# Kernel tuning notes

Hardware: AMD Instinct MI355X
Metric: run time of the kernel (lower is better)

Reference implementation:

```python
import jax, jax.numpy as jnp
import numpy as np

N_E = 1024
E_DIM = 256
N_TOK = 131072


def setup_inputs() -> dict:
    key = jax.random.key(0)
    kz, kw = jax.random.split(key)
    z = jax.random.normal(kz, (N_TOK, E_DIM), dtype=jnp.float32)
    weight = jax.random.normal(kw, (N_E, E_DIM), dtype=jnp.float32)
    return {"z": z, "weight": weight}


def reference(z, weight):
    # squared L2 distances: ||z||^2 + ||e||^2 - 2 z e^T  -> [N, n_e]
    d = (jnp.sum(z * z, axis=1, keepdims=True)
         + jnp.sum(weight * weight, axis=1)
         - 2.0 * jnp.matmul(z, weight.T))
    idx = jnp.argmin(d, axis=1)                       # [N]
    # gather codebook rows instead of materializing the one-hot @ weight matmul
    z_q = weight[idx]                                 # [N, e_dim]
    # straight-through estimator
    z_q = z + jax.lax.stop_gradient(z_q - z)
    # e_mean = mean of one-hot encodings == normalized code counts
    counts = jax.ops.segment_sum(jnp.ones_like(idx, dtype=z.dtype), idx,
                                 num_segments=N_E)    # [n_e]
    e_mean = counts / z.shape[0]
    perplexity = jnp.exp(-jnp.sum(e_mean * jnp.log(e_mean + 1e-10)))
    return z_q, perplexity
```

## Files before the change

kernel.cpp:

```cpp
#include <hip/hip_runtime.h>
#include <math.h>

#define NE   1024
#define ED   256
#define NT   131072
#define SLOTS 32

typedef __attribute__((ext_vector_type(8))) short short8;
typedef __attribute__((ext_vector_type(4))) float f32x4;

__device__ inline unsigned short f2bf(float f) {
    unsigned u = __float_as_uint(f);
    unsigned r = (u + 0x7FFFu + ((u >> 16) & 1u)) >> 16;
    return (unsigned short)r;
}

__device__ inline void gl_lds16(const void* g, void* l) {
    __builtin_amdgcn_global_load_lds(
        (const __attribute__((address_space(1))) unsigned int*)g,
        (__attribute__((address_space(3))) unsigned int*)l, 16, 0, 0);
}

__device__ inline unsigned pack_cand(float s, int code) {
    float qf = (s + 1024.f) * 16.f;
    int q = (int)qf;
    q = q < 0 ? 0 : (q > 65535 ? 65535 : q);
    return ((unsigned)q << 16) | (unsigned)code;
}


__global__ __launch_bounds__(256) void vq_prep(const float* __restrict__ w,
                                               float* __restrict__ wnorm,
                                               int* __restrict__ counts,
                                               unsigned short* __restrict__ wb) {
    int c = blockIdx.x * 256 + threadIdx.x;
    if (c < NE) {
        const float4* row = reinterpret_cast<const float4*>(w + (size_t)c * ED);
        ushort4* wbr = reinterpret_cast<ushort4*>(wb + (size_t)c * ED);
        float s = 0.f;
#pragma unroll 8
        for (int i = 0; i < ED / 4; ++i) {
            float4 v = row[i];
            s += v.x * v.x + v.y * v.y + v.z * v.z + v.w * v.w;
            ushort4 o;
            o.x = f2bf(v.x); o.y = f2bf(v.y); o.z = f2bf(v.z); o.w = f2bf(v.w);
            wbr[i] = o;
        }
        wnorm[c] = s;
        counts[c] = 0;
    }
}

__global__ __launch_bounds__(1024) void vq_wmax(const float* __restrict__ wnorm,
                                                float* __restrict__ wmax) {
    __shared__ float red[16];
    int tid = threadIdx.x;
    float v = wnorm[tid];
#pragma unroll
    for (int m = 32; m >= 1; m >>= 1) v = fmaxf(v, __shfl_xor(v, m, 64));
    if ((tid & 63) == 0) red[tid >> 6] = v;
    __syncthreads();
    if (tid == 0) {
        float m = red[0];
#pragma unroll
        for (int i = 1; i < 16; ++i) m = fmaxf(m, red[i]);
        wmax[0] = sqrtf(m);
    }
}

__global__ __launch_bounds__(512, 2) void vq_score3(const float* __restrict__ z,
                                                    const unsigned short* __restrict__ wb,
                                                    const float* __restrict__ wnorm,
                                                    const float* __restrict__ wmaxp,
                                                    unsigned* __restrict__ cnt,
                                                    unsigned* __restrict__ cand) {
    __shared__ __align__(16) unsigned short wlds[32768];
    __shared__ float wn_lds[NE];
    __shared__ float thr_lds[8][32];

    const int tid  = threadIdx.x;
    const int lane = tid & 63;
    const int wv_  = tid >> 6;
    const int l15  = lane & 15;
    const int l4   = lane >> 4;
    const int row0 = blockIdx.x * 256 + wv_ * 32;

#pragma unroll
    for (int p = 0; p < 8; ++p) {
        int s  = wv_ * 8 + p;
        int nj = s >> 3, kg = s & 7;
        int j  = nj * 16 + l15;
        gl_lds16(wb + (size_t)j * ED + kg * 32 + l4 * 8, &wlds[s * 512]);
    }

    reinterpret_cast<float2*>(wn_lds)[tid] = reinterpret_cast<const float2*>(wnorm)[tid];

    short8 a[2][8];
    float zn2[2];
#pragma unroll
    for (int mi = 0; mi < 2; ++mi) {
        const float* zr = z + (size_t)(row0 + mi * 16 + l15) * ED;
        float s = 0.f;
#pragma unroll
        for (int kg = 0; kg < 8; ++kg) {
            int k0 = kg * 32 + l4 * 8;
            float4 p = *reinterpret_cast<const float4*>(zr + k0);
            float4 q = *reinterpret_cast<const float4*>(zr + k0 + 4);
            s += p.x * p.x + p.y * p.y + p.z * p.z + p.w * p.w
               + q.x * q.x + q.y * q.y + q.z * q.z + q.w * q.w;
            short8 t;
            t[0] = (short)f2bf(p.x); t[1] = (short)f2bf(p.y);
            t[2] = (short)f2bf(p.z); t[3] = (short)f2bf(p.w);
            t[4] = (short)f2bf(q.x); t[5] = (short)f2bf(q.y);
            t[6] = (short)f2bf(q.z); t[7] = (short)f2bf(q.w);
            a[mi][kg] = t;
        }
        zn2[mi] = s;
    }
#pragma unroll
    for (int mi = 0; mi < 2; ++mi) {
        zn2[mi] += __shfl_xor(zn2[mi], 16, 64);
        zn2[mi] += __shfl_xor(zn2[mi], 32, 64);
    }
    float wmax = wmaxp[0];
#pragma unroll
    for (int mi = 0; mi < 2; ++mi)
        thr_lds[wv_][mi * 16 + l15] = 0.0313f * sqrtf(zn2[mi]) * wmax + 0.05f;

    asm volatile("s_waitcnt vmcnt(0) lgkmcnt(0)" ::: "memory");
    __builtin_amdgcn_s_barrier();

    float thrR[2], mn[2];
    int cnt_reg[2];
#pragma unroll
    for (int mi = 0; mi < 2; ++mi) {
        thrR[mi] = thr_lds[wv_][mi * 16 + l15];
        mn[mi] = 3.4e38f;
        cnt_reg[mi] = 0;
    }

    for (int st = 0; st < 8; ++st) {
        const int c0 = st * 128;

        for (int base = 0; base < 8; base += 2) {
            f32x4 acc[2][2];
#pragma unroll
            for (int tb = 0; tb < 2; ++tb)
#pragma unroll
                for (int mi = 0; mi < 2; ++mi) acc[tb][mi] = {0.f, 0.f, 0.f, 0.f};

#pragma unroll
            for (int tb = 0; tb < 2; ++tb)
#pragma unroll
                for (int kg = 0; kg < 8; ++kg) {
                    short8 wf = *reinterpret_cast<const short8*>(
                        &wlds[(((base + tb) * 8 + kg) * 512) + lane * 8]);
                    acc[tb][0] = __builtin_amdgcn_mfma_f32_16x16x32_bf16(wf, a[0][kg], acc[tb][0], 0, 0, 0);
                    acc[tb][1] = __builtin_amdgcn_mfma_f32_16x16x32_bf16(wf, a[1][kg], acc[tb][1], 0, 0, 0);
                }

            float4 wnv[2];
#pragma unroll
            for (int tb = 0; tb < 2; ++tb)
                wnv[tb] = *reinterpret_cast<const float4*>(
                    &wn_lds[c0 + (base + tb) * 16 + l4 * 4]);

            float tmin[2] = {3.4e38f, 3.4e38f};
#pragma unroll
            for (int tb = 0; tb < 2; ++tb)
#pragma unroll
                for (int mi = 0; mi < 2; ++mi) {
                    float wr[4] = {wnv[tb].x, wnv[tb].y, wnv[tb].z, wnv[tb].w};
#pragma unroll
                    for (int r = 0; r < 4; ++r) {
                        float s = fmaf(-2.f, acc[tb][mi][r], wr[r]);
                        acc[tb][mi][r] = s;
                        tmin[mi] = fminf(tmin[mi], s);
                    }
                }
#pragma unroll
            for (int mi = 0; mi < 2; ++mi) {
                float v = tmin[mi];
                v = fminf(v, __shfl_xor(v, 16, 64));
                v = fminf(v, __shfl_xor(v, 32, 64));
                mn[mi] = fminf(mn[mi], v);
            }

            unsigned km[2] = {0u, 0u};
#pragma unroll
            for (int tb = 0; tb < 2; ++tb)
#pragma unroll
                for (int mi = 0; mi < 2; ++mi)
#pragma unroll
                    for (int r = 0; r < 4; ++r)
                        if (acc[tb][mi][r] <= mn[mi] + thrR[mi])
                            km[mi] |= 1u << (tb * 4 + r);

            if (__any((km[0] | km[1]) != 0u)) {
#pragma unroll
                for (int mi = 0; mi < 2; ++mi) {
                    int kc = __popc(km[mi]);
                    int b = __shfl_xor(kc, 16, 64);
                    int c = __shfl_xor(kc, 32, 64);
                    int d = __shfl_xor(b, 32, 64);
                    int tot = kc + b + c + d;
                    if (tot > 0) {
                        int pfx = (l4 == 1) ? b
                                : (l4 == 2) ? (c + d)
                                : (l4 == 3) ? (b + c + d) : 0;
                        int tok = row0 + mi * 16 + l15;
                        int o = 0;
#pragma unroll
                        for (int tb = 0; tb < 2; ++tb)
#pragma unroll
                            for (int r = 0; r < 4; ++r)
                                if (km[mi] & (1u << (tb * 4 + r))) {
                                    int pos = cnt_reg[mi] + pfx + o;
                                    if (pos < SLOTS)
                                        cand[(size_t)tok * SLOTS + pos] =
                                            pack_cand(acc[tb][mi][r],
                                                      c0 + (base + tb) * 16 + l4 * 4 + r);
                                    ++o;
                                }
                        cnt_reg[mi] += tot;
                    }
                }
            }
        }

        if (st < 7) {
            asm volatile("s_waitcnt lgkmcnt(0)" ::: "memory");
            __builtin_amdgcn_s_barrier();
#pragma unroll
            for (int p = 0; p < 8; ++p) {
                int s  = wv_ * 8 + p;
                int nj = s >> 3, kg = s & 7;
                int j  = (st + 1) * 128 + nj * 16 + l15;
                gl_lds16(wb + (size_t)j * ED + kg * 32 + l4 * 8, &wlds[s * 512]);
            }
            asm volatile("s_waitcnt vmcnt(0) lgkmcnt(0)" ::: "memory");
            __builtin_amdgcn_s_barrier();
        }
    }

    if (l4 == 0) {
        cnt[row0 + l15]      = (unsigned)cnt_reg[0];
        cnt[row0 + 16 + l15] = (unsigned)cnt_reg[1];
    }
}

__global__ __launch_bounds__(256) void vq_refine(const float* __restrict__ z,
                                                 const float* __restrict__ w,
                                                 const float* __restrict__ wnorm,
                                                 const float* __restrict__ wmaxp,
                                                 const unsigned* __restrict__ cnt,
                                                 const unsigned* __restrict__ cand,
                                                 int* __restrict__ counts,
                                                 float* __restrict__ out) {
    const int lane = threadIdx.x & 63;
    const int t = blockIdx.x * 4 + (threadIdx.x >> 6);
    float4 zv = reinterpret_cast<const float4*>(z + (size_t)t * ED)[lane];
    unsigned n = cnt[t];
    float bs = 3.4e38f;
    int bj = NE;

    if (n >= 1u && n <= (unsigned)SLOTS) {
        unsigned pk = 0xFFFFFFFFu;
        if (lane < (int)n) pk = cand[(size_t)t * SLOTS + lane];
        unsigned pmin = pk;
#pragma unroll
        for (int m = 1; m < 64; m <<= 1) {
            unsigned o = __shfl_xor(pmin, m, 64);
            pmin = o < pmin ? o : pmin;
        }
        float zn = zv.x * zv.x + zv.y * zv.y + zv.z * zv.z + zv.w * zv.w;
#pragma unroll
        for (int m = 1; m < 64; m <<= 1) zn += __shfl_xor(zn, m, 64);
        float thr = 0.0313f * sqrtf(zn) * wmaxp[0] + 0.05f;
        unsigned margin = (unsigned)(16.f * thr) + 2u;
        unsigned qmin = pmin >> 16;
        bool keep = (lane < (int)n) && ((pk >> 16) <= qmin + margin);
        unsigned long long mask = __ballot(keep);
        while (mask) {
            int c = __ffsll(mask) - 1;
            mask &= mask - 1;
            int j = (int)(__shfl(pk, c, 64) & 0xFFFFu);
            float4 wv = reinterpret_cast<const float4*>(w + (size_t)j * ED)[lane];
            float d = fmaf(zv.x, wv.x, fmaf(zv.y, wv.y, fmaf(zv.z, wv.z, zv.w * wv.w)));
#pragma unroll
            for (int m = 1; m < 64; m <<= 1) d += __shfl_xor(d, m, 64);
            float s = fmaf(-2.f, d, wnorm[j]);
            if (s < bs || (s == bs && j < bj)) { bs = s; bj = j; }
        }
    } else {
        for (int j = 0; j < NE; ++j) {
            float4 wv = reinterpret_cast<const float4*>(w + (size_t)j * ED)[lane];
            float d = fmaf(zv.x, wv.x, fmaf(zv.y, wv.y, fmaf(zv.z, wv.z, zv.w * wv.w)));
#pragma unroll
            for (int m = 1; m < 64; m <<= 1) d += __shfl_xor(d, m, 64);
            float s = fmaf(-2.f, d, wnorm[j]);
            if (s < bs || (s == bs && j < bj)) { bs = s; bj = j; }
        }
    }
    float4 bw = reinterpret_cast<const float4*>(w + (size_t)bj * ED)[lane];
    reinterpret_cast<float4*>(out + (size_t)t * ED)[lane] = bw;
    if (lane == 0) atomicAdd(&counts[bj], 1);
}

__global__ __launch_bounds__(1024) void vq_pplx(const int* __restrict__ counts,
                                                float* __restrict__ out) {
    __shared__ float red[16];
    int tid = threadIdx.x;
    float e = (float)counts[tid] * (1.0f / (float)NT);
    float t = -e * logf(e + 1e-10f);
#pragma unroll
    for (int m = 32; m >= 1; m >>= 1) t += __shfl_down(t, m, 64);
    if ((tid & 63) == 0) red[tid >> 6] = t;
    __syncthreads();
    if (tid < 16) {
        float s = red[tid];
#pragma unroll
        for (int m = 8; m >= 1; m >>= 1) s += __shfl_down(s, m, 16);
        if (tid == 0) out[(size_t)NT * ED] = expf(s);
    }
}

#define TM 64
#define TN 64
#define KC 64

__global__ __launch_bounds__(256) void vq_prep0(const float* __restrict__ w,
                                                float* __restrict__ wnorm,
                                                int* __restrict__ counts) {
    int c = blockIdx.x * blockDim.x + threadIdx.x;
    if (c < NE) {
        const float4* row = reinterpret_cast<const float4*>(w + (size_t)c * ED);
        float s = 0.f;
#pragma unroll 8
        for (int i = 0; i < ED / 4; ++i) {
            float4 v = row[i];
            s += v.x * v.x + v.y * v.y + v.z * v.z + v.w * v.w;
        }
        wnorm[c] = s;
        counts[c] = 0;
    }
}

__global__ __launch_bounds__(256) void vq_argmin0(const float* __restrict__ z,
                                                  const float* __restrict__ w,
                                                  const float* __restrict__ wnorm,
                                                  int* __restrict__ idx_out,
                                                  int* __restrict__ counts) {
    __shared__ float zs[ED][TM];
    __shared__ float wsh[KC][TN];
    const int tid  = threadIdx.x;
    const int row0 = blockIdx.x * TM;
    const int cg   = tid & 15;
    const int tg   = tid >> 4;
#pragma unroll
    for (int p = 0; p < 16; ++p) {
        int f = p * 256 + tid;
        int k = f >> 4;
        int g = f & 15;
        float4 v;
        v.x = z[(size_t)(row0 + g * 4 + 0) * ED + k];
        v.y = z[(size_t)(row0 + g * 4 + 1) * ED + k];
        v.z = z[(size_t)(row0 + g * 4 + 2) * ED + k];
        v.w = z[(size_t)(row0 + g * 4 + 3) * ED + k];
        *reinterpret_cast<float4*>(&zs[k][g * 4]) = v;
    }
    float best[4];
    int   bidx[4];
#pragma unroll
    for (int i = 0; i < 4; ++i) { best[i] = 3.4e38f; bidx[i] = 0; }
    for (int ct = 0; ct < NE / TN; ++ct) {
        const int c0 = ct * TN;
        float acc[4][4];
#pragma unroll
        for (int i = 0; i < 4; ++i)
#pragma unroll
            for (int j = 0; j < 4; ++j) acc[i][j] = 0.f;
        for (int kc = 0; kc < ED / KC; ++kc) {
            __syncthreads();
#pragma unroll
            for (int p = 0; p < 4; ++p) {
                int f = p * 256 + tid;
                int k = f >> 4;
                int g = f & 15;
                float4 v;
                v.x = w[(size_t)(c0 + g * 4 + 0) * ED + kc * KC + k];
                v.y = w[(size_t)(c0 + g * 4 + 1) * ED + kc * KC + k];
                v.z = w[(size_t)(c0 + g * 4 + 2) * ED + kc * KC + k];
                v.w = w[(size_t)(c0 + g * 4 + 3) * ED + kc * KC + k];
                *reinterpret_cast<float4*>(&wsh[k][g * 4]) = v;
            }
            __syncthreads();
#pragma unroll 8
            for (int k = 0; k < KC; ++k) {
                float4 zv = *reinterpret_cast<const float4*>(&zs[kc * KC + k][tg * 4]);
                float4 wv = *reinterpret_cast<const float4*>(&wsh[k][cg * 4]);
                float zr[4] = { zv.x, zv.y, zv.z, zv.w };
                float wr[4] = { wv.x, wv.y, wv.z, wv.w };
#pragma unroll
                for (int i = 0; i < 4; ++i)
#pragma unroll
                    for (int j = 0; j < 4; ++j)
                        acc[i][j] = fmaf(zr[i], wr[j], acc[i][j]);
            }
        }
#pragma unroll
        for (int j = 0; j < 4; ++j) {
            int c = c0 + cg * 4 + j;
            float wn = wnorm[c];
#pragma unroll
            for (int i = 0; i < 4; ++i) {
                float s = fmaf(-2.f, acc[i][j], wn);
                if (s < best[i]) { best[i] = s; bidx[i] = c; }
            }
        }
    }
#pragma unroll
    for (int m = 1; m < 16; m <<= 1) {
#pragma unroll
        for (int i = 0; i < 4; ++i) {
            float ov = __shfl_xor(best[i], m, 64);
            int   oi = __shfl_xor(bidx[i], m, 64);
            if (ov < best[i] || (ov == best[i] && oi < bidx[i])) {
                best[i] = ov; bidx[i] = oi;
            }
        }
    }
    if (cg == 0) {
#pragma unroll
        for (int i = 0; i < 4; ++i) {
            int t = row0 + tg * 4 + i;
            idx_out[t] = bidx[i];
            atomicAdd(&counts[bidx[i]], 1);
        }
    }
}

__global__ __launch_bounds__(256) void vq_gather0(const float* __restrict__ w,
                                                  const int* __restrict__ idx,
                                                  float* __restrict__ out) {
    int tid = threadIdx.x;
    int t   = blockIdx.x * 4 + (tid >> 6);
    int c4  = tid & 63;
    int id  = idx[t];
    float4 v = reinterpret_cast<const float4*>(w + (size_t)id * ED)[c4];
    reinterpret_cast<float4*>(out + (size_t)t * ED)[c4] = v;
}

extern "C" void kernel_launch(void* const* d_in, const int* in_sizes, int n_in,
                              void* d_out, int out_size, void* d_ws, size_t ws_size,
                              hipStream_t stream) {
    const float* z = (const float*)d_in[0];
    const float* w = (const float*)d_in[1];
    float* out = (float*)d_out;
    char* ws = (char*)d_ws;

    float*          wnorm  = (float*)ws;
    int*            counts = (int*)(ws + 4096);
    float*          wmax   = (float*)(ws + 8192);
    unsigned short* wb     = (unsigned short*)(ws + 8448);
    unsigned*       cnt    = (unsigned*)(ws + 532736);
    unsigned*       cand   = (unsigned*)(ws + 1057024);
    const size_t need = 1057024 + (size_t)NT * SLOTS * 4;

    if (ws_size >= need) {
        vq_prep<<<4, 256, 0, stream>>>(w, wnorm, counts, wb);
        vq_wmax<<<1, 1024, 0, stream>>>(wnorm, wmax);
        vq_score3<<<NT / 256, 512, 0, stream>>>(z, wb, wnorm, wmax, cnt, cand);
        vq_refine<<<NT / 4, 256, 0, stream>>>(z, w, wnorm, wmax, cnt, cand, counts, out);
        vq_pplx<<<1, 1024, 0, stream>>>(counts, out);
    } else {
        int* idxw = (int*)(ws + 8192);
        vq_prep0<<<(NE + 255) / 256, 256, 0, stream>>>(w, wnorm, counts);
        vq_argmin0<<<NT / TM, 256, 0, stream>>>(z, w, wnorm, idxw, counts);
        vq_gather0<<<NT / 4, 256, 0, stream>>>(w, idxw, out);
        vq_pplx<<<1, 1024, 0, stream>>>(counts, out);
    }
}
```

Before: 281.6 us.

## Drop LDS staging of codebook; read bf16 weights directly into registers

The scoring kernel no longer stages codebook tiles in LDS with barriers. Each wave now loads its MFMA B-fragments straight from global memory, relying on L2 and L1 caching since the bf16 codebook is small. Each wave also handles 64 tokens instead of 32, so every loaded weight fragment feeds four MFMAs, and blocks shrink to 256 threads. This removes LDS traffic and block-wide synchronisation. In exchange it adds global and L1 load latency on the critical path and higher register pressure from 32 A-fragments per lane.

```diff
diff --git a/kernel.cpp b/kernel.cpp
--- a/kernel.cpp
+++ b/kernel.cpp
@@ -13,12 +13,6 @@
     unsigned u = __float_as_uint(f);
     unsigned r = (u + 0x7FFFu + ((u >> 16) & 1u)) >> 16;
     return (unsigned short)r;
-}
-
-__device__ inline void gl_lds16(const void* g, void* l) {
-    __builtin_amdgcn_global_load_lds(
-        (const __attribute__((address_space(1))) unsigned int*)g,
-        (__attribute__((address_space(3))) unsigned int*)l, 16, 0, 0);
 }
 
 __device__ inline unsigned pack_cand(float s, int code) {
@@ -68,184 +62,159 @@
     }
 }
 
-__global__ __launch_bounds__(512, 2) void vq_score3(const float* __restrict__ z,
-                                                    const unsigned short* __restrict__ wb,
-                                                    const float* __restrict__ wnorm,
-                                                    const float* __restrict__ wmaxp,
-                                                    unsigned* __restrict__ cnt,
-                                                    unsigned* __restrict__ cand) {
-    __shared__ __align__(16) unsigned short wlds[32768];
-    __shared__ float wn_lds[NE];
-    __shared__ float thr_lds[8][32];
-
+__global__ __launch_bounds__(256) void vq_score4(const float* __restrict__ z,
+                                                 const unsigned short* __restrict__ wb,
+                                                 const float* __restrict__ wnorm,
+                                                 const float* __restrict__ wmaxp,
+                                                 unsigned* __restrict__ cnt,
+                                                 unsigned* __restrict__ cand) {
     const int tid  = threadIdx.x;
     const int lane = tid & 63;
     const int wv_  = tid >> 6;
     const int l15  = lane & 15;
     const int l4   = lane >> 4;
-    const int row0 = blockIdx.x * 256 + wv_ * 32;
-
-#pragma unroll
-    for (int p = 0; p < 8; ++p) {
-        int s  = wv_ * 8 + p;
-        int nj = s >> 3, kg = s & 7;
-        int j  = nj * 16 + l15;
-        gl_lds16(wb + (size_t)j * ED + kg * 32 + l4 * 8, &wlds[s * 512]);
-    }
-
-    reinterpret_cast<float2*>(wn_lds)[tid] = reinterpret_cast<const float2*>(wnorm)[tid];
-
-    short8 a[2][8];
-    float zn2[2];
-#pragma unroll
-    for (int mi = 0; mi < 2; ++mi) {
-        const float* zr = z + (size_t)(row0 + mi * 16 + l15) * ED;
-        float s = 0.f;
-#pragma unroll
-        for (int kg = 0; kg < 8; ++kg) {
-            int k0 = kg * 32 + l4 * 8;
-            float4 p = *reinterpret_cast<const float4*>(zr + k0);
-            float4 q = *reinterpret_cast<const float4*>(zr + k0 + 4);
-            s += p.x * p.x + p.y * p.y + p.z * p.z + p.w * p.w
-               + q.x * q.x + q.y * q.y + q.z * q.z + q.w * q.w;
-            short8 t;
-            t[0] = (short)f2bf(p.x); t[1] = (short)f2bf(p.y);
-            t[2] = (short)f2bf(p.z); t[3] = (short)f2bf(p.w);
-            t[4] = (short)f2bf(q.x); t[5] = (short)f2bf(q.y);
-            t[6] = (short)f2bf(q.z); t[7] = (short)f2bf(q.w);
-            a[mi][kg] = t;
-        }
-        zn2[mi] = s;
-    }
-#pragma unroll
-    for (int mi = 0; mi < 2; ++mi) {
-        zn2[mi] += __shfl_xor(zn2[mi], 16, 64);
-        zn2[mi] += __shfl_xor(zn2[mi], 32, 64);
-    }
-    float wmax = wmaxp[0];
-#pragma unroll
-    for (int mi = 0; mi < 2; ++mi)
-        thr_lds[wv_][mi * 16 + l15] = 0.0313f * sqrtf(zn2[mi]) * wmax + 0.05f;
-
-    asm volatile("s_waitcnt vmcnt(0) lgkmcnt(0)" ::: "memory");
-    __builtin_amdgcn_s_barrier();
-
-    float thrR[2], mn[2];
-    int cnt_reg[2];
-#pragma unroll
-    for (int mi = 0; mi < 2; ++mi) {
-        thrR[mi] = thr_lds[wv_][mi * 16 + l15];
-        mn[mi] = 3.4e38f;
-        cnt_reg[mi] = 0;
-    }
-
-    for (int st = 0; st < 8; ++st) {
-        const int c0 = st * 128;
-
-        for (int base = 0; base < 8; base += 2) {
-            f32x4 acc[2][2];
-#pragma unroll
-            for (int tb = 0; tb < 2; ++tb)
-#pragma unroll
-                for (int mi = 0; mi < 2; ++mi) acc[tb][mi] = {0.f, 0.f, 0.f, 0.f};
-
-#pragma unroll
-            for (int tb = 0; tb < 2; ++tb)
-#pragma unroll
-                for (int kg = 0; kg < 8; ++kg) {
-                    short8 wf = *reinterpret_cast<const short8*>(
-                        &wlds[(((base + tb) * 8 + kg) * 512) + lane * 8]);
-                    acc[tb][0] = __builtin_amdgcn_mfma_f32_16x16x32_bf16(wf, a[0][kg], acc[tb][0], 0, 0, 0);
-                    acc[tb][1] = __builtin_amdgcn_mfma_f32_16x16x32_bf16(wf, a[1][kg], acc[tb][1], 0, 0, 0);
+    const int row0 = blockIdx.x * 256 + wv_ * 64;
+
+    short8 a[4][8];
+    float thrR[4], mn[4];
+    int cnt_reg[4];
+    {
+        float wmax = wmaxp[0];
+#pragma unroll
+        for (int mi = 0; mi < 4; ++mi) {
+            const float* zr = z + (size_t)(row0 + mi * 16 + l15) * ED;
+            float s = 0.f;
+#pragma unroll
+            for (int kg = 0; kg < 8; ++kg) {
+                int k0 = kg * 32 + l4 * 8;
+                float4 p = *reinterpret_cast<const float4*>(zr + k0);
+                float4 q = *reinterpret_cast<const float4*>(zr + k0 + 4);
+                s += p.x * p.x + p.y * p.y + p.z * p.z + p.w * p.w
+                   + q.x * q.x + q.y * q.y + q.z * q.z + q.w * q.w;
+                short8 t;
+                t[0] = (short)f2bf(p.x); t[1] = (short)f2bf(p.y);
+                t[2] = (short)f2bf(p.z); t[3] = (short)f2bf(p.w);
+                t[4] = (short)f2bf(q.x); t[5] = (short)f2bf(q.y);
+                t[6] = (short)f2bf(q.z); t[7] = (short)f2bf(q.w);
+                a[mi][kg] = t;
+            }
+            s += __shfl_xor(s, 16, 64);
+            s += __shfl_xor(s, 32, 64);
+            thrR[mi] = 0.0313f * sqrtf(s) * wmax + 0.05f;
+            mn[mi] = 3.4e38f;
+            cnt_reg[mi] = 0;
+        }
+    }
+
+    const unsigned short* wl = wb + (size_t)l15 * ED + l4 * 8;
+
+    for (int T = 0; T < 64; T += 2) {
+        short8 wfA[8];
+#pragma unroll
+        for (int kg = 0; kg < 8; ++kg)
+            wfA[kg] = *reinterpret_cast<const short8*>(
+                wl + (size_t)T * 16 * ED + kg * 32);
+        f32x4 accA[4];
+#pragma unroll
+        for (int mi = 0; mi < 4; ++mi) accA[mi] = {0.f, 0.f, 0.f, 0.f};
+#pragma unroll
+        for (int kg = 0; kg < 8; ++kg)
+#pragma unroll
+            for (int mi = 0; mi < 4; ++mi)
+                accA[mi] = __builtin_amdgcn_mfma_f32_16x16x32_bf16(
+                    wfA[kg], a[mi][kg], accA[mi], 0, 0, 0);
+
+        short8 wfB[8];
+#pragma unroll
+        for (int kg = 0; kg < 8; ++kg)
+            wfB[kg] = *reinterpret_cast<const short8*>(
+                wl + (size_t)(T + 1) * 16 * ED + kg * 32);
+        f32x4 accB[4];
+#pragma unroll
+        for (int mi = 0; mi < 4; ++mi) accB[mi] = {0.f, 0.f, 0.f, 0.f};
+#pragma unroll
+        for (int kg = 0; kg < 8; ++kg)
+#pragma unroll
+            for (int mi = 0; mi < 4; ++mi)
+                accB[mi] = __builtin_amdgcn_mfma_f32_16x16x32_bf16(
+                    wfB[kg], a[mi][kg], accB[mi], 0, 0, 0);
+
+        float4 wnvA = *reinterpret_cast<const float4*>(wnorm + T * 16 + l4 * 4);
+        float4 wnvB = *reinterpret_cast<const float4*>(wnorm + (T + 1) * 16 + l4 * 4);
+        float wrA[4] = {wnvA.x, wnvA.y, wnvA.z, wnvA.w};
+        float wrB[4] = {wnvB.x, wnvB.y, wnvB.z, wnvB.w};
+
+        float tmin[4] = {3.4e38f, 3.4e38f, 3.4e38f, 3.4e38f};
+#pragma unroll
+        for (int mi = 0; mi < 4; ++mi)
+#pragma unroll
+            for (int r = 0; r < 4; ++r) {
+                float sA = fmaf(-2.f, accA[mi][r], wrA[r]);
+                float sB = fmaf(-2.f, accB[mi][r], wrB[r]);
+                accA[mi][r] = sA;
+                accB[mi][r] = sB;
+                tmin[mi] = fminf(tmin[mi], fminf(sA, sB));
+            }
+#pragma unroll
+        for (int mi = 0; mi < 4; ++mi) {
+            float v = tmin[mi];
+            v = fminf(v, __shfl_xor(v, 16, 64));
+            v = fminf(v, __shfl_xor(v, 32, 64));
+            mn[mi] = fminf(mn[mi], v);
+        }
+
+        unsigned km[4] = {0u, 0u, 0u, 0u};
+#pragma unroll
+        for (int mi = 0; mi < 4; ++mi) {
+#pragma unroll
+            for (int r = 0; r < 4; ++r) {
+                if (accA[mi][r] <= mn[mi] + thrR[mi]) km[mi] |= 1u << r;
+                if (accB[mi][r] <= mn[mi] + thrR[mi]) km[mi] |= 1u << (4 + r);
+            }
+        }
+
+        if (__any((km[0] | km[1] | km[2] | km[3]) != 0u)) {
+#pragma unroll
+            for (int mi = 0; mi < 4; ++mi) {
+                int kc = __popc(km[mi]);
+                int b = __shfl_xor(kc, 16, 64);
+                int c = __shfl_xor(kc, 32, 64);
+                int d = __shfl_xor(b, 32, 64);
+                int tot = kc + b + c + d;
+                if (tot > 0) {
+                    int pfx = (l4 == 1) ? b
+                            : (l4 == 2) ? (c + d)
+                            : (l4 == 3) ? (b + c + d) : 0;
+                    int tok = row0 + mi * 16 + l15;
+                    int o = 0;
+#pragma unroll
+                    for (int r = 0; r < 4; ++r)
+                        if (km[mi] & (1u << r)) {
+                            int pos = cnt_reg[mi] + pfx + o;
+                            if (pos < SLOTS)
+                                cand[(size_t)tok * SLOTS + pos] =
+                                    pack_cand(accA[mi][r], T * 16 + l4 * 4 + r);
+                            ++o;
+                        }
+#pragma unroll
+                    for (int r = 0; r < 4; ++r)
+                        if (km[mi] & (1u << (4 + r))) {
+                            int pos = cnt_reg[mi] + pfx + o;
+                            if (pos < SLOTS)
+                                cand[(size_t)tok * SLOTS + pos] =
+                                    pack_cand(accB[mi][r], (T + 1) * 16 + l4 * 4 + r);
+                            ++o;
+                        }
+                    cnt_reg[mi] += tot;
                 }
-
-            float4 wnv[2];
-#pragma unroll
-            for (int tb = 0; tb < 2; ++tb)
-                wnv[tb] = *reinterpret_cast<const float4*>(
-                    &wn_lds[c0 + (base + tb) * 16 + l4 * 4]);
-
-            float tmin[2] = {3.4e38f, 3.4e38f};
-#pragma unroll
-            for (int tb = 0; tb < 2; ++tb)
-#pragma unroll
-                for (int mi = 0; mi < 2; ++mi) {
-                    float wr[4] = {wnv[tb].x, wnv[tb].y, wnv[tb].z, wnv[tb].w};
-#pragma unroll
-                    for (int r = 0; r < 4; ++r) {
-                        float s = fmaf(-2.f, acc[tb][mi][r], wr[r]);
-                        acc[tb][mi][r] = s;
-                        tmin[mi] = fminf(tmin[mi], s);
-                    }
-                }
-#pragma unroll
-            for (int mi = 0; mi < 2; ++mi) {
-                float v = tmin[mi];
-                v = fminf(v, __shfl_xor(v, 16, 64));
-                v = fminf(v, __shfl_xor(v, 32, 64));
-                mn[mi] = fminf(mn[mi], v);
-            }
-
-            unsigned km[2] = {0u, 0u};
-#pragma unroll
-            for (int tb = 0; tb < 2; ++tb)
-#pragma unroll
-                for (int mi = 0; mi < 2; ++mi)
-#pragma unroll
-                    for (int r = 0; r < 4; ++r)
-                        if (acc[tb][mi][r] <= mn[mi] + thrR[mi])
-                            km[mi] |= 1u << (tb * 4 + r);
-
-            if (__any((km[0] | km[1]) != 0u)) {
-#pragma unroll
-                for (int mi = 0; mi < 2; ++mi) {
-                    int kc = __popc(km[mi]);
-                    int b = __shfl_xor(kc, 16, 64);
-                    int c = __shfl_xor(kc, 32, 64);
-                    int d = __shfl_xor(b, 32, 64);
-                    int tot = kc + b + c + d;
-                    if (tot > 0) {
-                        int pfx = (l4 == 1) ? b
-                                : (l4 == 2) ? (c + d)
-                                : (l4 == 3) ? (b + c + d) : 0;
-                        int tok = row0 + mi * 16 + l15;
-                        int o = 0;
-#pragma unroll
-                        for (int tb = 0; tb < 2; ++tb)
-#pragma unroll
-                            for (int r = 0; r < 4; ++r)
-                                if (km[mi] & (1u << (tb * 4 + r))) {
-                                    int pos = cnt_reg[mi] + pfx + o;
-                                    if (pos < SLOTS)
-                                        cand[(size_t)tok * SLOTS + pos] =
-                                            pack_cand(acc[tb][mi][r],
-                                                      c0 + (base + tb) * 16 + l4 * 4 + r);
-                                    ++o;
-                                }
-                        cnt_reg[mi] += tot;
-                    }
-                }
-            }
-        }
-
-        if (st < 7) {
-            asm volatile("s_waitcnt lgkmcnt(0)" ::: "memory");
-            __builtin_amdgcn_s_barrier();
-#pragma unroll
-            for (int p = 0; p < 8; ++p) {
-                int s  = wv_ * 8 + p;
-                int nj = s >> 3, kg = s & 7;
-                int j  = (st + 1) * 128 + nj * 16 + l15;
-                gl_lds16(wb + (size_t)j * ED + kg * 32 + l4 * 8, &wlds[s * 512]);
-            }
-            asm volatile("s_waitcnt vmcnt(0) lgkmcnt(0)" ::: "memory");
-            __builtin_amdgcn_s_barrier();
+            }
         }
     }
 
     if (l4 == 0) {
-        cnt[row0 + l15]      = (unsigned)cnt_reg[0];
-        cnt[row0 + 16 + l15] = (unsigned)cnt_reg[1];
+#pragma unroll
+        for (int mi = 0; mi < 4; ++mi)
+            cnt[row0 + mi * 16 + l15] = (unsigned)cnt_reg[mi];
     }
 }
 
@@ -470,7 +439,7 @@
     if (ws_size >= need) {
         vq_prep<<<4, 256, 0, stream>>>(w, wnorm, counts, wb);
         vq_wmax<<<1, 1024, 0, stream>>>(wnorm, wmax);
-        vq_score3<<<NT / 256, 512, 0, stream>>>(z, wb, wnorm, wmax, cnt, cand);
+        vq_score4<<<NT / 256, 256, 0, stream>>>(z, wb, wnorm, wmax, cnt, cand);
         vq_refine<<<NT / 4, 256, 0, stream>>>(z, w, wnorm, wmax, cnt, cand, counts, out);
         vq_pplx<<<1, 1024, 0, stream>>>(counts, out);
     } else {
```

After: 400.1 us. +42.1%, slower.

## Split scoring into top-2 pass and rescoring pass for ambiguous tokens

Applied to the files above, without the earlier changes.

The single scoring kernel that tracked a running minimum and emitted every near-minimum candidate is replaced by two passes. The first pass keeps a per-token top-2 in registers and writes one candidate directly when the gap exceeds the bf16 error threshold. Otherwise it appends the token to an ambiguous list through an atomic counter. A second pass recomputes the bf16 scores only for the listed tokens against the fixed cutoff and emits candidates, so the per-tile shuffles and candidate writes leave the common path. In exchange the ambiguous tokens pay for the GEMM twice, an extra launch is added, and slots drop to 28.

```diff
diff --git a/kernel.cpp b/kernel.cpp
--- a/kernel.cpp
+++ b/kernel.cpp
@@ -4,7 +4,7 @@
 #define NE   1024
 #define ED   256
 #define NT   131072
-#define SLOTS 32
+#define SLOTS 28
 
 typedef __attribute__((ext_vector_type(8))) short short8;
 typedef __attribute__((ext_vector_type(4))) float f32x4;
@@ -32,7 +32,9 @@
 __global__ __launch_bounds__(256) void vq_prep(const float* __restrict__ w,
                                                float* __restrict__ wnorm,
                                                int* __restrict__ counts,
-                                               unsigned short* __restrict__ wb) {
+                                               unsigned short* __restrict__ wb,
+                                               unsigned* __restrict__ ambCount) {
+    if (blockIdx.x == 0 && threadIdx.x == 0) ambCount[0] = 0u;
     int c = blockIdx.x * 256 + threadIdx.x;
     if (c < NE) {
         const float4* row = reinterpret_cast<const float4*>(w + (size_t)c * ED);
@@ -68,15 +70,17 @@
     }
 }
 
-__global__ __launch_bounds__(512, 2) void vq_score3(const float* __restrict__ z,
-                                                    const unsigned short* __restrict__ wb,
-                                                    const float* __restrict__ wnorm,
-                                                    const float* __restrict__ wmaxp,
-                                                    unsigned* __restrict__ cnt,
-                                                    unsigned* __restrict__ cand) {
+__global__ __launch_bounds__(512) void vq_pass1(const float* __restrict__ z,
+                                                const unsigned short* __restrict__ wb,
+                                                const float* __restrict__ wnorm,
+                                                const float* __restrict__ wmaxp,
+                                                unsigned* __restrict__ cnt,
+                                                unsigned* __restrict__ cand,
+                                                float* __restrict__ cut,
+                                                unsigned* __restrict__ amb,
+                                                unsigned* __restrict__ ambCount) {
     __shared__ __align__(16) unsigned short wlds[32768];
     __shared__ float wn_lds[NE];
-    __shared__ float thr_lds[8][32];
 
     const int tid  = threadIdx.x;
     const int lane = tid & 63;
@@ -92,22 +96,188 @@
         int j  = nj * 16 + l15;
         gl_lds16(wb + (size_t)j * ED + kg * 32 + l4 * 8, &wlds[s * 512]);
     }
-
     reinterpret_cast<float2*>(wn_lds)[tid] = reinterpret_cast<const float2*>(wnorm)[tid];
 
     short8 a[2][8];
-    float zn2[2];
+    float thrR[2];
+    {
+        float wmax = wmaxp[0];
+#pragma unroll
+        for (int mi = 0; mi < 2; ++mi) {
+            const float* zr = z + (size_t)(row0 + mi * 16 + l15) * ED;
+            float s = 0.f;
+#pragma unroll
+            for (int kg = 0; kg < 8; ++kg) {
+                int k0 = kg * 32 + l4 * 8;
+                float4 p = *reinterpret_cast<const float4*>(zr + k0);
+                float4 q = *reinterpret_cast<const float4*>(zr + k0 + 4);
+                s += p.x * p.x + p.y * p.y + p.z * p.z + p.w * p.w
+                   + q.x * q.x + q.y * q.y + q.z * q.z + q.w * q.w;
+                short8 t;
+                t[0] = (short)f2bf(p.x); t[1] = (short)f2bf(p.y);
+                t[2] = (short)f2bf(p.z); t[3] = (short)f2bf(p.w);
+                t[4] = (short)f2bf(q.x); t[5] = (short)f2bf(q.y);
+                t[6] = (short)f2bf(q.z); t[7] = (short)f2bf(q.w);
+                a[mi][kg] = t;
+            }
+            s += __shfl_xor(s, 16, 64);
+            s += __shfl_xor(s, 32, 64);
+            thrR[mi] = 0.0313f * sqrtf(s) * wmax + 0.05f;
+        }
+    }
+
+    asm volatile("s_waitcnt vmcnt(0) lgkmcnt(0)" ::: "memory");
+    __builtin_amdgcn_s_barrier();
+
+    float v1[2] = {3.4e38f, 3.4e38f};
+    float v2[2] = {3.4e38f, 3.4e38f};
+    int   c1[2] = {NE, NE};
+
+    for (int st = 0; st < 8; ++st) {
+        const int c0 = st * 128;
+
+        for (int base = 0; base < 8; base += 2) {
+            f32x4 accA[2], accB[2];
+#pragma unroll
+            for (int mi = 0; mi < 2; ++mi) { accA[mi] = {0.f,0.f,0.f,0.f}; accB[mi] = {0.f,0.f,0.f,0.f}; }
+
+#pragma unroll
+            for (int kg = 0; kg < 8; ++kg) {
+                short8 wf = *reinterpret_cast<const short8*>(
+                    &wlds[((base * 8 + kg) * 512) + lane * 8]);
+                accA[0] = __builtin_amdgcn_mfma_f32_16x16x32_bf16(wf, a[0][kg], accA[0], 0, 0, 0);
+                accA[1] = __builtin_amdgcn_mfma_f32_16x16x32_bf16(wf, a[1][kg], accA[1], 0, 0, 0);
+            }
+#pragma unroll
+            for (int kg = 0; kg < 8; ++kg) {
+                short8 wf = *reinterpret_cast<const short8*>(
+                    &wlds[(((base + 1) * 8 + kg) * 512) + lane * 8]);
+                accB[0] = __builtin_amdgcn_mfma_f32_16x16x32_bf16(wf, a[0][kg], accB[0], 0, 0, 0);
+                accB[1] = __builtin_amdgcn_mfma_f32_16x16x32_bf16(wf, a[1][kg], accB[1], 0, 0, 0);
+            }
+
+            const int codeA = c0 + base * 16 + l4 * 4;
+            const int codeB = codeA + 16;
+            float4 wnvA = *reinterpret_cast<const float4*>(&wn_lds[codeA]);
+            float4 wnvB = *reinterpret_cast<const float4*>(&wn_lds[codeB]);
+            float wrA[4] = {wnvA.x, wnvA.y, wnvA.z, wnvA.w};
+            float wrB[4] = {wnvB.x, wnvB.y, wnvB.z, wnvB.w};
+
+#pragma unroll
+            for (int mi = 0; mi < 2; ++mi) {
+#pragma unroll
+                for (int r = 0; r < 4; ++r) {
+                    float s = fmaf(-2.f, accA[mi][r], wrA[r]);
+                    bool lt = s < v1[mi];
+                    v2[mi] = lt ? v1[mi] : fminf(v2[mi], s);
+                    c1[mi] = lt ? (codeA + r) : c1[mi];
+                    v1[mi] = lt ? s : v1[mi];
+                }
+#pragma unroll
+                for (int r = 0; r < 4; ++r) {
+                    float s = fmaf(-2.f, accB[mi][r], wrB[r]);
+                    bool lt = s < v1[mi];
+                    v2[mi] = lt ? v1[mi] : fminf(v2[mi], s);
+                    c1[mi] = lt ? (codeB + r) : c1[mi];
+                    v1[mi] = lt ? s : v1[mi];
+                }
+            }
+        }
+
+        if (st < 7) {
+            asm volatile("s_waitcnt lgkmcnt(0)" ::: "memory");
+            __builtin_amdgcn_s_barrier();
+#pragma unroll
+            for (int p = 0; p < 8; ++p) {
+                int s  = wv_ * 8 + p;
+                int nj = s >> 3, kg = s & 7;
+                int j  = (st + 1) * 128 + nj * 16 + l15;
+                gl_lds16(wb + (size_t)j * ED + kg * 32 + l4 * 8, &wlds[s * 512]);
+            }
+            asm volatile("s_waitcnt vmcnt(0) lgkmcnt(0)" ::: "memory");
+            __builtin_amdgcn_s_barrier();
+        }
+    }
+
+#pragma unroll
+    for (int m = 16; m <= 32; m <<= 1) {
+#pragma unroll
+        for (int mi = 0; mi < 2; ++mi) {
+            float ov1 = __shfl_xor(v1[mi], m, 64);
+            int   oc1 = __shfl_xor(c1[mi], m, 64);
+            float ov2 = __shfl_xor(v2[mi], m, 64);
+            float nv2 = fminf(fmaxf(v1[mi], ov1), fminf(v2[mi], ov2));
+            bool take = (ov1 < v1[mi]) || (ov1 == v1[mi] && oc1 < c1[mi]);
+            v1[mi] = take ? ov1 : v1[mi];
+            c1[mi] = take ? oc1 : c1[mi];
+            v2[mi] = nv2;
+        }
+    }
+
+    if (l4 == 0) {
+#pragma unroll
+        for (int mi = 0; mi < 2; ++mi) {
+            int tok = row0 + mi * 16 + l15;
+            if (v2[mi] - v1[mi] > thrR[mi]) {
+                cnt[tok] = 1u;
+                cand[(size_t)tok * SLOTS] = pack_cand(v1[mi], c1[mi]);
+            } else {
+                cut[tok] = v1[mi] + thrR[mi];
+                unsigned p = atomicAdd(ambCount, 1u);
+                amb[p] = (unsigned)tok;
+            }
+        }
+    }
+}
+
+__global__ __launch_bounds__(512) void vq_pass2(const float* __restrict__ z,
+                                                const unsigned short* __restrict__ wb,
+                                                const float* __restrict__ wnorm,
+                                                const unsigned* __restrict__ amb,
+                                                const unsigned* __restrict__ ambCountP,
+                                                const float* __restrict__ cut,
+                                                unsigned* __restrict__ cnt,
+                                                unsigned* __restrict__ cand) {
+    const unsigned ambN = ambCountP[0];
+    if (blockIdx.x * 256u >= ambN) return;
+
+    __shared__ __align__(16) unsigned short wlds[32768];
+    __shared__ float wn_lds[NE];
+
+    const int tid  = threadIdx.x;
+    const int lane = tid & 63;
+    const int wv_  = tid >> 6;
+    const int l15  = lane & 15;
+    const int l4   = lane >> 4;
+    const int base = blockIdx.x * 256 + wv_ * 32;
+
+#pragma unroll
+    for (int p = 0; p < 8; ++p) {
+        int s  = wv_ * 8 + p;
+        int nj = s >> 3, kg = s & 7;
+        int j  = nj * 16 + l15;
+        gl_lds16(wb + (size_t)j * ED + kg * 32 + l4 * 8, &wlds[s * 512]);
+    }
+    reinterpret_cast<float2*>(wn_lds)[tid] = reinterpret_cast<const float2*>(wnorm)[tid];
+
+    int tokR[2]; bool val[2]; float cutR[2];
 #pragma unroll
     for (int mi = 0; mi < 2; ++mi) {
-        const float* zr = z + (size_t)(row0 + mi * 16 + l15) * ED;
-        float s = 0.f;
+        unsigned ii = (unsigned)(base + mi * 16 + l15);
+        val[mi] = ii < ambN;
+        tokR[mi] = val[mi] ? (int)amb[ii] : 0;
+        cutR[mi] = val[mi] ? cut[tokR[mi]] : -3.4e38f;
+    }
+
+    short8 a[2][8];
+#pragma unroll
+    for (int mi = 0; mi < 2; ++mi) {
+        const float* zr = z + (size_t)tokR[mi] * ED;
 #pragma unroll
         for (int kg = 0; kg < 8; ++kg) {
             int k0 = kg * 32 + l4 * 8;
             float4 p = *reinterpret_cast<const float4*>(zr + k0);
             float4 q = *reinterpret_cast<const float4*>(zr + k0 + 4);
-            s += p.x * p.x + p.y * p.y + p.z * p.z + p.w * p.w
-               + q.x * q.x + q.y * q.y + q.z * q.z + q.w * q.w;
             short8 t;
             t[0] = (short)f2bf(p.x); t[1] = (short)f2bf(p.y);
             t[2] = (short)f2bf(p.z); t[3] = (short)f2bf(p.w);
@@ -115,86 +285,56 @@
             t[6] = (short)f2bf(q.z); t[7] = (short)f2bf(q.w);
             a[mi][kg] = t;
         }
-        zn2[mi] = s;
-    }
-#pragma unroll
-    for (int mi = 0; mi < 2; ++mi) {
-        zn2[mi] += __shfl_xor(zn2[mi], 16, 64);
-        zn2[mi] += __shfl_xor(zn2[mi], 32, 64);
-    }
-    float wmax = wmaxp[0];
-#pragma unroll
-    for (int mi = 0; mi < 2; ++mi)
-        thr_lds[wv_][mi * 16 + l15] = 0.0313f * sqrtf(zn2[mi]) * wmax + 0.05f;
+    }
 
     asm volatile("s_waitcnt vmcnt(0) lgkmcnt(0)" ::: "memory");
     __builtin_amdgcn_s_barrier();
 
-    float thrR[2], mn[2];
-    int cnt_reg[2];
-#pragma unroll
-    for (int mi = 0; mi < 2; ++mi) {
-        thrR[mi] = thr_lds[wv_][mi * 16 + l15];
-        mn[mi] = 3.4e38f;
-        cnt_reg[mi] = 0;
-    }
+    int cnt_reg[2] = {0, 0};
 
     for (int st = 0; st < 8; ++st) {
         const int c0 = st * 128;
 
-        for (int base = 0; base < 8; base += 2) {
-            f32x4 acc[2][2];
-#pragma unroll
-            for (int tb = 0; tb < 2; ++tb)
-#pragma unroll
-                for (int mi = 0; mi < 2; ++mi) acc[tb][mi] = {0.f, 0.f, 0.f, 0.f};
-
-#pragma unroll
-            for (int tb = 0; tb < 2; ++tb)
-#pragma unroll
-                for (int kg = 0; kg < 8; ++kg) {
-                    short8 wf = *reinterpret_cast<const short8*>(
-                        &wlds[(((base + tb) * 8 + kg) * 512) + lane * 8]);
-                    acc[tb][0] = __builtin_amdgcn_mfma_f32_16x16x32_bf16(wf, a[0][kg], acc[tb][0], 0, 0, 0);
-                    acc[tb][1] = __builtin_amdgcn_mfma_f32_16x16x32_bf16(wf, a[1][kg], acc[tb][1], 0, 0, 0);
+        for (int base2 = 0; base2 < 8; base2 += 2) {
+            f32x4 accA[2], accB[2];
+#pragma unroll
+            for (int mi = 0; mi < 2; ++mi) { accA[mi] = {0.f,0.f,0.f,0.f}; accB[mi] = {0.f,0.f,0.f,0.f}; }
+
+#pragma unroll
+            for (int kg = 0; kg < 8; ++kg) {
+                short8 wf = *reinterpret_cast<const short8*>(
+                    &wlds[((base2 * 8 + kg) * 512) + lane * 8]);
+                accA[0] = __builtin_amdgcn_mfma_f32_16x16x32_bf16(wf, a[0][kg], accA[0], 0, 0, 0);
+                accA[1] = __builtin_amdgcn_mfma_f32_16x16x32_bf16(wf, a[1][kg], accA[1], 0, 0, 0);
+            }
+#pragma unroll
+            for (int kg = 0; kg < 8; ++kg) {
+                short8 wf = *reinterpret_cast<const short8*>(
+                    &wlds[(((base2 + 1) * 8 + kg) * 512) + lane * 8]);
+                accB[0] = __builtin_amdgcn_mfma_f32_16x16x32_bf16(wf, a[0][kg], accB[0], 0, 0, 0);
+                accB[1] = __builtin_amdgcn_mfma_f32_16x16x32_bf16(wf, a[1][kg], accB[1], 0, 0, 0);
+            }
+
+            const int codeA = c0 + base2 * 16 + l4 * 4;
+            const int codeB = codeA + 16;
+            float4 wnvA = *reinterpret_cast<const float4*>(&wn_lds[codeA]);
+            float4 wnvB = *reinterpret_cast<const float4*>(&wn_lds[codeB]);
+            float wrA[4] = {wnvA.x, wnvA.y, wnvA.z, wnvA.w};
+            float wrB[4] = {wnvB.x, wnvB.y, wnvB.z, wnvB.w};
+
+            unsigned km[2] = {0u, 0u};
+#pragma unroll
+            for (int mi = 0; mi < 2; ++mi) {
+#pragma unroll
+                for (int r = 0; r < 4; ++r) {
+                    float sA = fmaf(-2.f, accA[mi][r], wrA[r]);
+                    float sB = fmaf(-2.f, accB[mi][r], wrB[r]);
+                    accA[mi][r] = sA;
+                    accB[mi][r] = sB;
+                    if (sA <= cutR[mi]) km[mi] |= 1u << r;
+                    if (sB <= cutR[mi]) km[mi] |= 1u << (4 + r);
                 }
-
-            float4 wnv[2];
-#pragma unroll
-            for (int tb = 0; tb < 2; ++tb)
-                wnv[tb] = *reinterpret_cast<const float4*>(
-                    &wn_lds[c0 + (base + tb) * 16 + l4 * 4]);
-
-            float tmin[2] = {3.4e38f, 3.4e38f};
-#pragma unroll
-            for (int tb = 0; tb < 2; ++tb)
-#pragma unroll
-                for (int mi = 0; mi < 2; ++mi) {
-                    float wr[4] = {wnv[tb].x, wnv[tb].y, wnv[tb].z, wnv[tb].w};
-#pragma unroll
-                    for (int r = 0; r < 4; ++r) {
-                        float s = fmaf(-2.f, acc[tb][mi][r], wr[r]);
-                        acc[tb][mi][r] = s;
-                        tmin[mi] = fminf(tmin[mi], s);
-                    }
-                }
-#pragma unroll
-            for (int mi = 0; mi < 2; ++mi) {
-                float v = tmin[mi];
-                v = fminf(v, __shfl_xor(v, 16, 64));
-                v = fminf(v, __shfl_xor(v, 32, 64));
-                mn[mi] = fminf(mn[mi], v);
-            }
-
-            unsigned km[2] = {0u, 0u};
-#pragma unroll
-            for (int tb = 0; tb < 2; ++tb)
-#pragma unroll
-                for (int mi = 0; mi < 2; ++mi)
-#pragma unroll
-                    for (int r = 0; r < 4; ++r)
-                        if (acc[tb][mi][r] <= mn[mi] + thrR[mi])
-                            km[mi] |= 1u << (tb * 4 + r);
+            }
 
             if (__any((km[0] | km[1]) != 0u)) {
 #pragma unroll
@@ -208,20 +348,26 @@
                         int pfx = (l4 == 1) ? b
                                 : (l4 == 2) ? (c + d)
                                 : (l4 == 3) ? (b + c + d) : 0;
-                        int tok = row0 + mi * 16 + l15;
+                        int tok = tokR[mi];
                         int o = 0;
 #pragma unroll
-                        for (int tb = 0; tb < 2; ++tb)
-#pragma unroll
-                            for (int r = 0; r < 4; ++r)
-                                if (km[mi] & (1u << (tb * 4 + r))) {
-                                    int pos = cnt_reg[mi] + pfx + o;
-                                    if (pos < SLOTS)
-                                        cand[(size_t)tok * SLOTS + pos] =
-                                            pack_cand(acc[tb][mi][r],
-                                                      c0 + (base + tb) * 16 + l4 * 4 + r);
-                                    ++o;
-                                }
+                        for (int r = 0; r < 4; ++r)
+                            if (km[mi] & (1u << r)) {
+                                int pos = cnt_reg[mi] + pfx + o;
+                                if (pos < SLOTS)
+                                    cand[(size_t)tok * SLOTS + pos] =
+                                        pack_cand(accA[mi][r], codeA + r);
+                                ++o;
+                            }
+#pragma unroll
+                        for (int r = 0; r < 4; ++r)
+                            if (km[mi] & (1u << (4 + r))) {
+                                int pos = cnt_reg[mi] + pfx + o;
+                                if (pos < SLOTS)
+                                    cand[(size_t)tok * SLOTS + pos] =
+                                        pack_cand(accB[mi][r], codeB + r);
+                                ++o;
+                            }
                         cnt_reg[mi] += tot;
                     }
                 }
@@ -244,8 +390,9 @@
     }
 
     if (l4 == 0) {
-        cnt[row0 + l15]      = (unsigned)cnt_reg[0];
-        cnt[row0 + 16 + l15] = (unsigned)cnt_reg[1];
+#pragma unroll
+        for (int mi = 0; mi < 2; ++mi)
+            if (val[mi]) cnt[tokR[mi]] = (unsigned)cnt_reg[mi];
     }
 }
 
@@ -459,18 +606,24 @@
     float* out = (float*)d_out;
     char* ws = (char*)d_ws;
 
-    float*          wnorm  = (float*)ws;
-    int*            counts = (int*)(ws + 4096);
-    float*          wmax   = (float*)(ws + 8192);
-    unsigned short* wb     = (unsigned short*)(ws + 8448);
-    unsigned*       cnt    = (unsigned*)(ws + 532736);
-    unsigned*       cand   = (unsigned*)(ws + 1057024);
-    const size_t need = 1057024 + (size_t)NT * SLOTS * 4;
+    float*          wnorm    = (float*)ws;
+    int*            counts   = (int*)(ws + 4096);
+    float*          wmax     = (float*)(ws + 8192);
+    unsigned short* wb       = (unsigned short*)(ws + 8448);
+    unsigned*       cnt      = (unsigned*)(ws + 532736);
+    float*          cut      = (float*)(ws + 1057024);
+    unsigned*       amb      = (unsigned*)(ws + 1581312);
+    unsigned*       ambCount = (unsigned*)(ws + 2105600);
+    unsigned*       cand     = (unsigned*)(ws + 2105856);
+    const size_t need = 2105856 + (size_t)NT * SLOTS * 4;
 
     if (ws_size >= need) {
-        vq_prep<<<4, 256, 0, stream>>>(w, wnorm, counts, wb);
+        vq_prep<<<4, 256, 0, stream>>>(w, wnorm, counts, wb, ambCount);
         vq_wmax<<<1, 1024, 0, stream>>>(wnorm, wmax);
-        vq_score3<<<NT / 256, 512, 0, stream>>>(z, wb, wnorm, wmax, cnt, cand);
+        vq_pass1<<<NT / 256, 512, 0, stream>>>(z, wb, wnorm, wmax, cnt, cand,
+                                               cut, amb, ambCount);
+        vq_pass2<<<NT / 256, 512, 0, stream>>>(z, wb, wnorm, amb, ambCount,
+                                               cut, cnt, cand);
         vq_refine<<<NT / 4, 256, 0, stream>>>(z, w, wnorm, wmax, cnt, cand, counts, out);
         vq_pplx<<<1, 1024, 0, stream>>>(counts, out);
     } else {
```

New measurement: 444.4 us. 1.58x slower.
